# Kernel optimization log

Hardware: AMD Instinct MI355X
Metric: run time of the kernel (lower is better)

Reference implementation:

```python
import jax, jax.numpy as jnp
import numpy as np

N_HEAD = 16
N_STATE = 1024
NEG_INF = -1e9


def setup_inputs() -> dict:
    key = jax.random.key(0)
    k1, = jax.random.split(key, 1)
    B, S = 4, 2048
    x = jax.random.normal(k1, (B, S, 3 * N_STATE), dtype=jnp.float32)
    # causal attention mask (1 = keep, 0 = masked), broadcast over heads
    attn_mask = jnp.tril(jnp.ones((S, S), dtype=jnp.float32))[None, None, :, :]
    attn_mask = jnp.broadcast_to(attn_mask, (B, 1, S, S))
    return {"x": x, "attn_mask": attn_mask}


def reference(x, attn_mask) -> jnp.ndarray:
    B, S, _ = x.shape
    d_head = N_STATE // N_HEAD
    q = x[:, :, :N_STATE].reshape(B, S, N_HEAD, d_head).transpose(0, 2, 1, 3)  # [B,H,S,D]
    k = x[:, :, N_STATE:2 * N_STATE].reshape(B, S, N_HEAD, d_head).transpose(0, 2, 1, 3)
    v = x[:, :, 2 * N_STATE:].reshape(B, S, N_HEAD, d_head).transpose(0, 2, 1, 3)
    scale = 1.0 / jnp.sqrt(jnp.asarray(d_head, dtype=x.dtype))
    w = jnp.einsum('bhqd,bhkd->bhqk', q, k) * scale           # [B,H,S,S]
    w = attn_mask * w + (1.0 - attn_mask) * NEG_INF
    w = jax.nn.softmax(w, axis=-1)
    # attention_dropout is identity at inference (Keras Dropout, training=False)
    a = jnp.einsum('bhqk,bhkd->bhqd', w, v)                   # [B,H,S,D]
    return a.transpose(0, 2, 1, 3).reshape(B, S, N_STATE)
```

## Files before the change

kernel.cpp:

```cpp
#include <hip/hip_runtime.h>


typedef float  f32x4   __attribute__((ext_vector_type(4)));
typedef float  f32x16  __attribute__((ext_vector_type(16)));
typedef short  bf16x8  __attribute__((ext_vector_type(8)));

#define NH      16
#define DH      64
#define SEQ     2048
#define NSTATE  1024
#define ROW3    3072
#define BQ      256
#define BK      64
#define NQB     (SEQ / BQ)
#define KST     72
#define VST     72
#define NEG_BIG (-1e9f)
#define QSC     (0.125f * 1.4426950408889634f)

static __device__ __forceinline__ unsigned pk2(float x, float y) {
    unsigned ux = __builtin_bit_cast(unsigned, x);
    unsigned uy = __builtin_bit_cast(unsigned, y);
    ux += 0x7FFFu + ((ux >> 16) & 1u);
    uy += 0x7FFFu + ((uy >> 16) & 1u);
    return __builtin_amdgcn_perm(uy, ux, 0x07060302u);
}

#define ISSUE_STAGE(KV0)                                                       \
    {                                                                          \
        _Pragma("unroll")                                                      \
        for (int i = 0; i < 2; ++i) {                                          \
            int p  = tid + 512 * i;                                            \
            int kv = p >> 4;                                                   \
            int d  = (p & 15) * 4;                                             \
            kp[i] = *(const f32x4*)(kbase + (size_t)((KV0) + kv) * ROW3 + d);  \
        }                                                                      \
        _Pragma("unroll")                                                      \
        for (int i = 0; i < 4; ++i) {                                          \
            int d  = (tid & 15) + 16 * i;                                      \
            int kv = (tid >> 4) * 2;                                           \
            const float* gp = vbase + (size_t)((KV0) + kv) * ROW3 + d;         \
            vp[2 * i]     = gp[0];                                             \
            vp[2 * i + 1] = gp[ROW3];                                          \
        }                                                                      \
    }

#define COMMIT_STAGE(BUF)                                                      \
    {                                                                          \
        _Pragma("unroll")                                                      \
        for (int i = 0; i < 2; ++i) {                                          \
            int p  = tid + 512 * i;                                            \
            int kv = p >> 4;                                                   \
            int d  = (p & 15) * 4;                                             \
            uint2 w;                                                           \
            w.x = pk2(kp[i][0], kp[i][1]);                                     \
            w.y = pk2(kp[i][2], kp[i][3]);                                     \
            *(uint2*)&Klds[BUF][kv * KST + d] = w;                             \
        }                                                                      \
        _Pragma("unroll")                                                      \
        for (int i = 0; i < 4; ++i) {                                          \
            int d  = (tid & 15) + 16 * i;                                      \
            int kv = (tid >> 4) * 2;                                           \
            *(unsigned*)&Vlds[BUF][d * VST + kv] = pk2(vp[2 * i], vp[2 * i + 1]); \
        }                                                                      \
    }

__global__ __launch_bounds__(512, 2)
void mha_fwd(const float* __restrict__ x, float* __restrict__ out) {
    const int tid  = threadIdx.x;
    const int wave = tid >> 6;
    const int lane = tid & 63;
    const int r31  = lane & 31;
    const int hl   = lane >> 5;

    const int bid = blockIdx.x;
    const int pr  = bid >> 6;
    const int bh  = bid & 63;
    const int b   = bh >> 4;
    const int h   = bh & 15;

    const float* xb    = x + (size_t)b * SEQ * ROW3;
    const float* kbase = xb + NSTATE + h * DH;
    const float* vbase = xb + 2 * NSTATE + h * DH;
    float*       ob    = out + (size_t)b * SEQ * NSTATE + h * DH;

    __shared__ __align__(16) short Klds[2][BK * KST];
    __shared__ __align__(16) short Vlds[2][DH * VST];

    f32x4 kp[2];
    float vp[8];

#pragma unroll 1
    for (int ph = 0; ph < 2; ++ph) {
        const int qblk   = ph ? (NQB - 1 - pr) : pr;
        const int q0     = qblk * BQ;
        const int qstrip = q0 + wave * 32;
        const int qrow   = qstrip + r31;

        bf16x8 qf[4];
        {
            const float* qp = xb + (size_t)qrow * ROW3 + h * DH + hl * 8;
#pragma unroll
            for (int kc = 0; kc < 4; ++kc) {
                f32x4 a = *(const f32x4*)(qp + 16 * kc);
                f32x4 c = *(const f32x4*)(qp + 16 * kc + 4);
                union { bf16x8 v; unsigned u[4]; } qq;
                qq.u[0] = pk2(a[0] * QSC, a[1] * QSC);
                qq.u[1] = pk2(a[2] * QSC, a[3] * QSC);
                qq.u[2] = pk2(c[0] * QSC, c[1] * QSC);
                qq.u[3] = pk2(c[2] * QSC, c[3] * QSC);
                qf[kc] = qq.v;
            }
        }

        f32x16 o0, o1;
#pragma unroll
        for (int r = 0; r < 16; ++r) { o0[r] = 0.f; o1[r] = 0.f; }
        float dl = 0.f;

        const int ntiles = q0 / BK + BQ / BK;

        __syncthreads();
        ISSUE_STAGE(0)
        COMMIT_STAGE(0)
        __syncthreads();

#pragma unroll 1
        for (int it = 0; it < ntiles; ++it) {
            const int kv0 = it * BK;
            const int cur = it & 1;
            const bool pf = (it + 1 < ntiles);

            if (pf) ISSUE_STAGE((it + 1) * BK)

            if (kv0 <= qstrip + 31) {
#pragma unroll
                for (int H = 0; H < 2; ++H) {
                    const int kvb = kv0 + 32 * H;
                    if (kvb <= qstrip + 31) {
                        bf16x8 kf[4];
#pragma unroll
                        for (int kc = 0; kc < 4; ++kc)
                            kf[kc] = *(const bf16x8*)&Klds[cur][(32 * H + r31) * KST + 16 * kc + 8 * hl];

                        f32x16 s;
#pragma unroll
                        for (int r = 0; r < 16; ++r) s[r] = 0.f;
#pragma unroll
                        for (int kc = 0; kc < 4; ++kc)
                            s = __builtin_amdgcn_mfma_f32_32x32x16_bf16(kf[kc], qf[kc], s, 0, 0, 0);

                        if (kvb + 31 > qstrip) {
#pragma unroll
                            for (int r = 0; r < 16; ++r) {
                                int kvg = kvb + (r & 3) + 8 * (r >> 2) + 4 * hl;
                                if (kvg > qrow) s[r] = NEG_BIG;
                            }
                        }
#pragma unroll
                        for (int r = 0; r < 16; ++r)
                            s[r] = __builtin_amdgcn_exp2f(s[r]);

                        {
                            float a0 = (s[0] + s[1]) + (s[2] + s[3]);
                            float a1 = (s[4] + s[5]) + (s[6] + s[7]);
                            float a2 = (s[8] + s[9]) + (s[10] + s[11]);
                            float a3 = (s[12] + s[13]) + (s[14] + s[15]);
                            dl += (a0 + a1) + (a2 + a3);
                        }

#pragma unroll
                        for (int cc = 0; cc < 2; ++cc) {
                            unsigned wA = pk2(s[8 * cc + 0], s[8 * cc + 1]);
                            unsigned wB = pk2(s[8 * cc + 2], s[8 * cc + 3]);
                            unsigned wC = pk2(s[8 * cc + 4], s[8 * cc + 5]);
                            unsigned wD = pk2(s[8 * cc + 6], s[8 * cc + 7]);
                            __asm__ volatile("v_permlane32_swap_b32 %0, %1"
                                             : "+v"(wA), "+v"(wC));
                            __asm__ volatile("v_permlane32_swap_b32 %0, %1"
                                             : "+v"(wB), "+v"(wD));
                            union { bf16x8 v; unsigned u[4]; } pa;
                            pa.u[0] = wA; pa.u[1] = wB; pa.u[2] = wC; pa.u[3] = wD;

                            const int c = 2 * H + cc;
                            bf16x8 vf0 = *(const bf16x8*)&Vlds[cur][(r31)      * VST + 16 * c + 8 * hl];
                            bf16x8 vf1 = *(const bf16x8*)&Vlds[cur][(32 + r31) * VST + 16 * c + 8 * hl];
                            o0 = __builtin_amdgcn_mfma_f32_32x32x16_bf16(pa.v, vf0, o0, 0, 0, 0);
                            o1 = __builtin_amdgcn_mfma_f32_32x32x16_bf16(pa.v, vf1, o1, 0, 0, 0);
                        }
                    }
                }
            }

            if (pf) COMMIT_STAGE(cur ^ 1)
            __syncthreads();
        }

        {
            unsigned da = __builtin_bit_cast(unsigned, dl);
            unsigned db = da;
            __asm__ volatile("v_permlane32_swap_b32 %0, %1" : "+v"(da), "+v"(db));
            float dtot = __builtin_bit_cast(float, da) + __builtin_bit_cast(float, db);
            float rcp  = 1.0f / dtot;
#pragma unroll
            for (int r = 0; r < 16; ++r) {
                int srcq = (r & 3) + 8 * (r >> 2) + 4 * hl;
                float lr = __builtin_bit_cast(float,
                    __builtin_amdgcn_ds_bpermute(srcq << 2,
                        __builtin_bit_cast(int, rcp)));
                const size_t row = (size_t)(qstrip + srcq) * NSTATE;
                ob[row + r31]      = o0[r] * lr;
                ob[row + 32 + r31] = o1[r] * lr;
            }
        }
    }
}

extern "C" void kernel_launch(void* const* d_in, const int* in_sizes, int n_in,
                              void* d_out, int out_size, void* d_ws, size_t ws_size,
                              hipStream_t stream) {
    const float* x = (const float*)d_in[0];
    float* out = (float*)d_out;
    dim3 grid(4 * NH * (NQB / 2));
    dim3 block(512);
    hipLaunchKernelGGL(mha_fwd, grid, block, 0, stream, x, out);
}
```

Measured before the change: 219.1 us.

## Split each KV tile across two wave groups with 1024-thread blocks and LDS reduction

Doubles the block to 1024 threads (16 waves). Each query strip is now handled by two waves, and each of the two waves processes one 32-key half of every 64-key tile. The partial output accumulators and denominators are combined through an LDS scratch pool at the end of each phase, with each wave writing half of the output columns. This is meant to raise wave-level parallelism and latency hiding, and s_setprio is added around the MFMA groups. In exchange it adds extra LDS traffic, two more barriers per phase, and register pressure under launch_bounds(1024,4).

```diff
diff --git a/kernel.cpp b/kernel.cpp
--- a/kernel.cpp
+++ b/kernel.cpp
@@ -18,6 +18,10 @@
 #define NEG_BIG (-1e9f)
 #define QSC     (0.125f * 1.4426950408889634f)
 
+#define KOFF(buf)  ((buf) * (BK * KST))
+#define VOFF(buf)  (2 * BK * KST + (buf) * (DH * VST))
+#define POOLSZ     34816
+
 static __device__ __forceinline__ unsigned pk2(float x, float y) {
     unsigned ux = __builtin_bit_cast(unsigned, x);
     unsigned uy = __builtin_bit_cast(unsigned, y);
@@ -28,50 +32,53 @@
 
 #define ISSUE_STAGE(KV0)                                                       \
     {                                                                          \
-        _Pragma("unroll")                                                      \
-        for (int i = 0; i < 2; ++i) {                                          \
-            int p  = tid + 512 * i;                                            \
-            int kv = p >> 4;                                                   \
-            int d  = (p & 15) * 4;                                             \
-            kp[i] = *(const f32x4*)(kbase + (size_t)((KV0) + kv) * ROW3 + d);  \
-        }                                                                      \
-        _Pragma("unroll")                                                      \
-        for (int i = 0; i < 4; ++i) {                                          \
-            int d  = (tid & 15) + 16 * i;                                      \
-            int kv = (tid >> 4) * 2;                                           \
-            const float* gp = vbase + (size_t)((KV0) + kv) * ROW3 + d;         \
-            vp[2 * i]     = gp[0];                                             \
-            vp[2 * i + 1] = gp[ROW3];                                          \
+        {                                                                      \
+            int kv = tid >> 4;                                                 \
+            int d  = (tid & 15) * 4;                                           \
+            kp0 = *(const f32x4*)(kbase + (size_t)((KV0) + kv) * ROW3 + d);    \
+        }                                                                      \
+        if (tid < 512) {                                                       \
+            _Pragma("unroll")                                                  \
+            for (int i = 0; i < 4; ++i) {                                      \
+                int d  = (tid & 15) + 16 * i;                                  \
+                int kv = (tid >> 4) * 2;                                       \
+                const float* gp = vbase + (size_t)((KV0) + kv) * ROW3 + d;     \
+                vp[2 * i]     = gp[0];                                         \
+                vp[2 * i + 1] = gp[ROW3];                                      \
+            }                                                                  \
         }                                                                      \
     }
 
 #define COMMIT_STAGE(BUF)                                                      \
     {                                                                          \
-        _Pragma("unroll")                                                      \
-        for (int i = 0; i < 2; ++i) {                                          \
-            int p  = tid + 512 * i;                                            \
-            int kv = p >> 4;                                                   \
-            int d  = (p & 15) * 4;                                             \
+        {                                                                      \
+            int kv = tid >> 4;                                                 \
+            int d  = (tid & 15) * 4;                                           \
             uint2 w;                                                           \
-            w.x = pk2(kp[i][0], kp[i][1]);                                     \
-            w.y = pk2(kp[i][2], kp[i][3]);                                     \
-            *(uint2*)&Klds[BUF][kv * KST + d] = w;                             \
-        }                                                                      \
-        _Pragma("unroll")                                                      \
-        for (int i = 0; i < 4; ++i) {                                          \
-            int d  = (tid & 15) + 16 * i;                                      \
-            int kv = (tid >> 4) * 2;                                           \
-            *(unsigned*)&Vlds[BUF][d * VST + kv] = pk2(vp[2 * i], vp[2 * i + 1]); \
+            w.x = pk2(kp0[0], kp0[1]);                                         \
+            w.y = pk2(kp0[2], kp0[3]);                                         \
+            *(uint2*)&POOL[KOFF(BUF) + kv * KST + d] = w;                      \
+        }                                                                      \
+        if (tid < 512) {                                                       \
+            _Pragma("unroll")                                                  \
+            for (int i = 0; i < 4; ++i) {                                      \
+                int d  = (tid & 15) + 16 * i;                                  \
+                int kv = (tid >> 4) * 2;                                       \
+                *(unsigned*)&POOL[VOFF(BUF) + d * VST + kv] =                  \
+                    pk2(vp[2 * i], vp[2 * i + 1]);                             \
+            }                                                                  \
         }                                                                      \
     }
 
-__global__ __launch_bounds__(512, 2)
+__global__ __launch_bounds__(1024, 4)
 void mha_fwd(const float* __restrict__ x, float* __restrict__ out) {
-    const int tid  = threadIdx.x;
-    const int wave = tid >> 6;
-    const int lane = tid & 63;
-    const int r31  = lane & 31;
-    const int hl   = lane >> 5;
+    const int tid   = threadIdx.x;
+    const int wave  = tid >> 6;
+    const int lane  = tid & 63;
+    const int r31   = lane & 31;
+    const int hl    = lane >> 5;
+    const int strip = wave & 7;
+    const int kvh   = wave >> 3;
 
     const int bid = blockIdx.x;
     const int pr  = bid >> 6;
@@ -84,17 +91,16 @@
     const float* vbase = xb + 2 * NSTATE + h * DH;
     float*       ob    = out + (size_t)b * SEQ * NSTATE + h * DH;
 
-    __shared__ __align__(16) short Klds[2][BK * KST];
-    __shared__ __align__(16) short Vlds[2][DH * VST];
-
-    f32x4 kp[2];
+    __shared__ __align__(16) short POOL[POOLSZ];
+
+    f32x4 kp0;
     float vp[8];
 
 #pragma unroll 1
     for (int ph = 0; ph < 2; ++ph) {
         const int qblk   = ph ? (NQB - 1 - pr) : pr;
         const int q0     = qblk * BQ;
-        const int qstrip = q0 + wave * 32;
+        const int qstrip = q0 + strip * 32;
         const int qrow   = qstrip + r31;
 
         bf16x8 qf[4];
@@ -133,75 +139,89 @@
 
             if (pf) ISSUE_STAGE((it + 1) * BK)
 
-            if (kv0 <= qstrip + 31) {
-#pragma unroll
-                for (int H = 0; H < 2; ++H) {
-                    const int kvb = kv0 + 32 * H;
-                    if (kvb <= qstrip + 31) {
-                        bf16x8 kf[4];
-#pragma unroll
-                        for (int kc = 0; kc < 4; ++kc)
-                            kf[kc] = *(const bf16x8*)&Klds[cur][(32 * H + r31) * KST + 16 * kc + 8 * hl];
-
-                        f32x16 s;
-#pragma unroll
-                        for (int r = 0; r < 16; ++r) s[r] = 0.f;
-#pragma unroll
-                        for (int kc = 0; kc < 4; ++kc)
-                            s = __builtin_amdgcn_mfma_f32_32x32x16_bf16(kf[kc], qf[kc], s, 0, 0, 0);
-
-                        if (kvb + 31 > qstrip) {
-#pragma unroll
-                            for (int r = 0; r < 16; ++r) {
-                                int kvg = kvb + (r & 3) + 8 * (r >> 2) + 4 * hl;
-                                if (kvg > qrow) s[r] = NEG_BIG;
-                            }
-                        }
-#pragma unroll
-                        for (int r = 0; r < 16; ++r)
-                            s[r] = __builtin_amdgcn_exp2f(s[r]);
-
-                        {
-                            float a0 = (s[0] + s[1]) + (s[2] + s[3]);
-                            float a1 = (s[4] + s[5]) + (s[6] + s[7]);
-                            float a2 = (s[8] + s[9]) + (s[10] + s[11]);
-                            float a3 = (s[12] + s[13]) + (s[14] + s[15]);
-                            dl += (a0 + a1) + (a2 + a3);
-                        }
-
-#pragma unroll
-                        for (int cc = 0; cc < 2; ++cc) {
-                            unsigned wA = pk2(s[8 * cc + 0], s[8 * cc + 1]);
-                            unsigned wB = pk2(s[8 * cc + 2], s[8 * cc + 3]);
-                            unsigned wC = pk2(s[8 * cc + 4], s[8 * cc + 5]);
-                            unsigned wD = pk2(s[8 * cc + 6], s[8 * cc + 7]);
-                            __asm__ volatile("v_permlane32_swap_b32 %0, %1"
-                                             : "+v"(wA), "+v"(wC));
-                            __asm__ volatile("v_permlane32_swap_b32 %0, %1"
-                                             : "+v"(wB), "+v"(wD));
-                            union { bf16x8 v; unsigned u[4]; } pa;
-                            pa.u[0] = wA; pa.u[1] = wB; pa.u[2] = wC; pa.u[3] = wD;
-
-                            const int c = 2 * H + cc;
-                            bf16x8 vf0 = *(const bf16x8*)&Vlds[cur][(r31)      * VST + 16 * c + 8 * hl];
-                            bf16x8 vf1 = *(const bf16x8*)&Vlds[cur][(32 + r31) * VST + 16 * c + 8 * hl];
-                            o0 = __builtin_amdgcn_mfma_f32_32x32x16_bf16(pa.v, vf0, o0, 0, 0, 0);
-                            o1 = __builtin_amdgcn_mfma_f32_32x32x16_bf16(pa.v, vf1, o1, 0, 0, 0);
-                        }
+            const int kvb = kv0 + 32 * kvh;
+            if (kvb <= qstrip + 31) {
+                bf16x8 kf[4];
+#pragma unroll
+                for (int kc = 0; kc < 4; ++kc)
+                    kf[kc] = *(const bf16x8*)&POOL[KOFF(cur) + (32 * kvh + r31) * KST + 16 * kc + 8 * hl];
+
+                f32x16 s;
+#pragma unroll
+                for (int r = 0; r < 16; ++r) s[r] = 0.f;
+                __builtin_amdgcn_s_setprio(1);
+#pragma unroll
+                for (int kc = 0; kc < 4; ++kc)
+                    s = __builtin_amdgcn_mfma_f32_32x32x16_bf16(kf[kc], qf[kc], s, 0, 0, 0);
+                __builtin_amdgcn_s_setprio(0);
+
+                if (kvb + 31 > qstrip) {
+#pragma unroll
+                    for (int r = 0; r < 16; ++r) {
+                        int kvg = kvb + (r & 3) + 8 * (r >> 2) + 4 * hl;
+                        if (kvg > qrow) s[r] = NEG_BIG;
                     }
                 }
+#pragma unroll
+                for (int r = 0; r < 16; ++r)
+                    s[r] = __builtin_amdgcn_exp2f(s[r]);
+
+                {
+                    float a0 = (s[0] + s[1]) + (s[2] + s[3]);
+                    float a1 = (s[4] + s[5]) + (s[6] + s[7]);
+                    float a2 = (s[8] + s[9]) + (s[10] + s[11]);
+                    float a3 = (s[12] + s[13]) + (s[14] + s[15]);
+                    dl += (a0 + a1) + (a2 + a3);
+                }
+
+#pragma unroll
+                for (int cc = 0; cc < 2; ++cc) {
+                    unsigned wA = pk2(s[8 * cc + 0], s[8 * cc + 1]);
+                    unsigned wB = pk2(s[8 * cc + 2], s[8 * cc + 3]);
+                    unsigned wC = pk2(s[8 * cc + 4], s[8 * cc + 5]);
+                    unsigned wD = pk2(s[8 * cc + 6], s[8 * cc + 7]);
+                    __asm__ volatile("v_permlane32_swap_b32 %0, %1"
+                                     : "+v"(wA), "+v"(wC));
+                    __asm__ volatile("v_permlane32_swap_b32 %0, %1"
+                                     : "+v"(wB), "+v"(wD));
+                    union { bf16x8 v; unsigned u[4]; } pa;
+                    pa.u[0] = wA; pa.u[1] = wB; pa.u[2] = wC; pa.u[3] = wD;
+
+                    const int c = 2 * kvh + cc;
+                    bf16x8 vf0 = *(const bf16x8*)&POOL[VOFF(cur) + (r31)      * VST + 16 * c + 8 * hl];
+                    bf16x8 vf1 = *(const bf16x8*)&POOL[VOFF(cur) + (32 + r31) * VST + 16 * c + 8 * hl];
+                    __builtin_amdgcn_s_setprio(1);
+                    o0 = __builtin_amdgcn_mfma_f32_32x32x16_bf16(pa.v, vf0, o0, 0, 0, 0);
+                    o1 = __builtin_amdgcn_mfma_f32_32x32x16_bf16(pa.v, vf1, o1, 0, 0, 0);
+                    __builtin_amdgcn_s_setprio(0);
+                }
             }
 
             if (pf) COMMIT_STAGE(cur ^ 1)
             __syncthreads();
         }
 
+        float dtot;
         {
             unsigned da = __builtin_bit_cast(unsigned, dl);
             unsigned db = da;
             __asm__ volatile("v_permlane32_swap_b32 %0, %1" : "+v"(da), "+v"(db));
-            float dtot = __builtin_bit_cast(float, da) + __builtin_bit_cast(float, db);
-            float rcp  = 1.0f / dtot;
+            dtot = __builtin_bit_cast(float, da) + __builtin_bit_cast(float, db);
+        }
+        {
+            float* scr = (float*)POOL;
+            const int wbase = ((strip << 1) | kvh) * (17 * 64) + lane * 17;
+#pragma unroll
+            for (int j = 0; j < 16; ++j)
+                scr[wbase + j] = kvh ? o0[j] : o1[j];
+            scr[wbase + 16] = dtot;
+            __syncthreads();
+            const int rbase = ((strip << 1) | (kvh ^ 1)) * (17 * 64) + lane * 17;
+            float po[16];
+#pragma unroll
+            for (int j = 0; j < 16; ++j) po[j] = scr[rbase + j];
+            float pd  = scr[rbase + 16];
+            float rcp = 1.0f / (dtot + pd);
 #pragma unroll
             for (int r = 0; r < 16; ++r) {
                 int srcq = (r & 3) + 8 * (r >> 2) + 4 * hl;
@@ -209,9 +229,10 @@
                     __builtin_amdgcn_ds_bpermute(srcq << 2,
                         __builtin_bit_cast(int, rcp)));
                 const size_t row = (size_t)(qstrip + srcq) * NSTATE;
-                ob[row + r31]      = o0[r] * lr;
-                ob[row + 32 + r31] = o1[r] * lr;
+                if (kvh == 0) ob[row + r31]      = (o0[r] + po[r]) * lr;
+                else          ob[row + 32 + r31] = (o1[r] + po[r]) * lr;
             }
+            __syncthreads();
         }
     }
 }
@@ -222,6 +243,6 @@
     const float* x = (const float*)d_in[0];
     float* out = (float*)d_out;
     dim3 grid(4 * NH * (NQB / 2));
-    dim3 block(512);
+    dim3 block(1024);
     hipLaunchKernelGGL(mha_fwd, grid, block, 0, stream, x, out);
 }
```

Result: slower. 230.2 us (+5.1%).
